# Performance work log

Hardware: AMD Instinct MI355X
Metric: run time of the kernel (lower is better)

## Reference

```python
import jax, jax.numpy as jnp
import numpy as np

B, N, H, HEADS, F, L = 32, 256, 512, 8, 2048, 8
D = H // HEADS  # per-head dim
EPS = 1e-5


def _layernorm(x, scale, bias):
    mu = jnp.mean(x, axis=-1, keepdims=True)
    var = jnp.mean(jnp.square(x - mu), axis=-1, keepdims=True)
    return (x - mu) * jax.lax.rsqrt(var + EPS) * scale + bias


def setup_inputs() -> dict:
    key = jax.random.key(0)
    ks = jax.random.split(key, 12)
    s = 0.02
    inp = {
        "x": jax.random.normal(ks[0], (B, N, H), jnp.float32),
        "attn_bias": jax.random.normal(ks[1], (B, HEADS, N, N), jnp.float32),
        "ln1_s": jnp.ones((L, H), jnp.float32),
        "ln1_b": jnp.zeros((L, H), jnp.float32),
        "wq": s * jax.random.normal(ks[2], (L, H, H), jnp.float32),
        "bq": jnp.zeros((L, H), jnp.float32),
        "wk": s * jax.random.normal(ks[3], (L, H, H), jnp.float32),
        "bk": jnp.zeros((L, H), jnp.float32),
        "wv": s * jax.random.normal(ks[4], (L, H, H), jnp.float32),
        "bv": jnp.zeros((L, H), jnp.float32),
        "wo": s * jax.random.normal(ks[5], (L, H, H), jnp.float32),
        "bo": jnp.zeros((L, H), jnp.float32),
        "ln2_s": jnp.ones((L, H), jnp.float32),
        "ln2_b": jnp.zeros((L, H), jnp.float32),
        "w1": s * jax.random.normal(ks[6], (L, H, F), jnp.float32),
        "b1": jnp.zeros((L, F), jnp.float32),
        "w2": s * jax.random.normal(ks[7], (L, F, H), jnp.float32),
        "b2": jnp.zeros((L, H), jnp.float32),
    }
    return inp


def reference(x, attn_bias, ln1_s, ln1_b, wq, bq, wk, bk, wv, bv, wo, bo,
              ln2_s, ln2_b, w1, b1, w2, b2):
    scale = D ** (-0.5)
    for l in range(L):
        # --- self attention block ---
        y = _layernorm(x, ln1_s[l], ln1_b[l])
        q = (y @ wq[l] + bq[l]).reshape(B, N, HEADS, D) * scale
        k = (y @ wk[l] + bk[l]).reshape(B, N, HEADS, D)
        v = (y @ wv[l] + bv[l]).reshape(B, N, HEADS, D)
        scores = jnp.einsum("bqhd,bkhd->bhqk", q, k) + attn_bias
        probs = jax.nn.softmax(scores, axis=-1)
        ctx = jnp.einsum("bhqk,bkhd->bqhd", probs, v).reshape(B, N, H)
        x = x + ctx @ wo[l] + bo[l]
        # --- FFN block ---
        y = _layernorm(x, ln2_s[l], ln2_b[l])
        y = jax.nn.gelu(y @ w1[l] + b1[l], approximate=False)
        x = x + y @ w2[l] + b2[l]
    return x
```

## Files before the change

### kernel.cpp

```cpp
#include <hip/hip_runtime.h>
#include <hip/hip_bf16.h>
#include <math.h>

typedef __bf16 bf16;
typedef __bf16 bf16x8 __attribute__((ext_vector_type(8)));
typedef float  f32x4  __attribute__((ext_vector_type(4)));

#define DEV __device__ __forceinline__

DEV f32x4 mfma16(bf16x8 a, bf16x8 b, f32x4 c) {
    return __builtin_amdgcn_mfma_f32_16x16x32_bf16(a, b, c, 0, 0, 0);
}

template <int MODE>
__global__ __launch_bounds__(256, 2) void gemm_k(
    const bf16* __restrict__ A, const bf16* __restrict__ Bt,
    const float* __restrict__ bias, bf16* __restrict__ Cb,
    float* __restrict__ Cf, int K, int ldC)
{
    __shared__ bf16 As[128 * 32];
    __shared__ bf16 Bs[128 * 32];
    const int tid  = threadIdx.x;
    const int lane = tid & 63;
    const int w    = tid >> 6;
    const int wm   = w & 1, wn = w >> 1;
    const long tm  = (long)blockIdx.y * 128;
    const long tn  = (long)blockIdx.x * 128;

    f32x4 acc[4][4] = {};

    const int p0 = tid, p1 = tid + 256;
    const int r0 = p0 >> 2, c0 = (p0 & 3) * 8;
    const int r1 = p1 >> 2, c1 = (p1 & 3) * 8;
    const bf16* A0 = A + (tm + r0) * K + c0;
    const bf16* A1 = A + (tm + r1) * K + c1;
    const bf16* B0 = Bt + (tn + r0) * K + c0;
    const bf16* B1 = Bt + (tn + r1) * K + c1;

    int am[4], bn[4];
#pragma unroll
    for (int i = 0; i < 4; ++i) {
        int ra = wm * 64 + i * 16 + (lane & 15);
        am[i]  = ra * 32 + (lane >> 4) * 8;
        int rb = wn * 64 + i * 16 + (lane & 15);
        bn[i]  = rb * 32 + (lane >> 4) * 8;
    }

    for (int k0 = 0; k0 < K; k0 += 32) {
        uint4 va0 = *(const uint4*)(A0 + k0);
        uint4 va1 = *(const uint4*)(A1 + k0);
        uint4 vb0 = *(const uint4*)(B0 + k0);
        uint4 vb1 = *(const uint4*)(B1 + k0);
        __syncthreads();
        *(uint4*)&As[p0 * 8] = va0;
        *(uint4*)&As[p1 * 8] = va1;
        *(uint4*)&Bs[p0 * 8] = vb0;
        *(uint4*)&Bs[p1 * 8] = vb1;
        __syncthreads();
        bf16x8 a[4], b[4];
#pragma unroll
        for (int i = 0; i < 4; ++i) a[i] = *(const bf16x8*)&As[am[i]];
#pragma unroll
        for (int i = 0; i < 4; ++i) b[i] = *(const bf16x8*)&Bs[bn[i]];
#pragma unroll
        for (int mi = 0; mi < 4; ++mi)
#pragma unroll
            for (int ni = 0; ni < 4; ++ni)
                acc[mi][ni] = mfma16(a[mi], b[ni], acc[mi][ni]);
    }

#pragma unroll
    for (int mi = 0; mi < 4; ++mi) {
        const long rbase = tm + wm * 64 + mi * 16 + ((lane >> 4) << 2);
#pragma unroll
        for (int ni = 0; ni < 4; ++ni) {
            const long col = tn + wn * 64 + ni * 16 + (lane & 15);
            const float bv = bias[col];
#pragma unroll
            for (int r = 0; r < 4; ++r) {
                float v = acc[mi][ni][r] + bv;
                if constexpr (MODE == 1)
                    v = 0.5f * v * (1.0f + erff(v * 0.70710678118654752f));
                const long idx = (rbase + r) * (long)ldC + col;
                if constexpr (MODE == 2) Cf[idx] += v;
                else                     Cb[idx] = (bf16)v;
            }
        }
    }
}

__global__ __launch_bounds__(256, 2) void attn_k(
    const bf16* __restrict__ qkv, const float* __restrict__ bias,
    bf16* __restrict__ ctx)
{
    __shared__ bf16 smem[256 * 72 + 32 * 264];
    bf16* Ks = smem;
    bf16* Vt = smem + 256 * 72;

    const int tid = threadIdx.x, lane = tid & 63, w = tid >> 6;
    const int qt = blockIdx.x & 3;
    const int h  = (blockIdx.x >> 2) & 7;
    const int b  = blockIdx.x >> 5;
    const long qkv_base = (long)b * 256 * 1536;

#pragma unroll
    for (int i = 0; i < 8; ++i) {
        int p = i * 256 + tid;
        int n = p >> 3, kk = (p & 7) * 8;
        uint4 v = *(const uint4*)(qkv + qkv_base + (long)n * 1536 + 512 + h * 64 + kk);
        *(uint4*)&Ks[n * 72 + kk] = v;
    }
    {
        int d = tid & 31, nb = tid >> 5;
#pragma unroll 4
        for (int i = 0; i < 32; ++i) {
            int n = nb + i * 8;
            Vt[d * 264 + n] = qkv[qkv_base + (long)n * 1536 + 1024 + h * 64 + d];
        }
    }

    const int qr0 = qt * 64 + w * 16;
    bf16x8 aq0, aq1;
    {
        const bf16* g = qkv + qkv_base + (long)(qr0 + (lane & 15)) * 1536 + h * 64 + ((lane >> 4) * 8);
        aq0 = *(const bf16x8*)g;
        aq1 = *(const bf16x8*)(g + 32);
    }
    __syncthreads();

    f32x4 s[16];
    const float* bb = bias + (((long)(b * 8 + h)) * 256 + qr0) * 256;
#pragma unroll
    for (int ct = 0; ct < 16; ++ct) {
        const int col = ct * 16 + (lane & 15);
        f32x4 c;
#pragma unroll
        for (int r = 0; r < 4; ++r)
            c[r] = bb[(long)((lane >> 4) * 4 + r) * 256 + col];
        bf16x8 k0 = *(const bf16x8*)&Ks[(ct * 16 + (lane & 15)) * 72 + ((lane >> 4) * 8)];
        bf16x8 k1 = *(const bf16x8*)&Ks[(ct * 16 + (lane & 15)) * 72 + 32 + ((lane >> 4) * 8)];
        c = mfma16(aq0, k0, c);
        c = mfma16(aq1, k1, c);
        s[ct] = c;
    }

    float m[4] = {-1e30f, -1e30f, -1e30f, -1e30f};
#pragma unroll
    for (int ct = 0; ct < 16; ++ct)
#pragma unroll
        for (int r = 0; r < 4; ++r) m[r] = fmaxf(m[r], s[ct][r]);
#pragma unroll
    for (int r = 0; r < 4; ++r)
#pragma unroll
        for (int off = 1; off < 16; off <<= 1)
            m[r] = fmaxf(m[r], __shfl_xor(m[r], off));
    float l[4] = {0.f, 0.f, 0.f, 0.f};
#pragma unroll
    for (int ct = 0; ct < 16; ++ct)
#pragma unroll
        for (int r = 0; r < 4; ++r) {
            float p = __expf(s[ct][r] - m[r]);
            s[ct][r] = p;
            l[r] += p;
        }
#pragma unroll
    for (int r = 0; r < 4; ++r) {
#pragma unroll
        for (int off = 1; off < 16; off <<= 1) l[r] += __shfl_xor(l[r], off);
        l[r] = 1.0f / l[r];
    }

    __syncthreads();
    bf16* P = Ks + w * (16 * 264);
#pragma unroll
    for (int ct = 0; ct < 16; ++ct)
#pragma unroll
        for (int r = 0; r < 4; ++r)
            P[(long)((lane >> 4) * 4 + r) * 264 + ct * 16 + (lane & 15)] = (bf16)s[ct][r];

    bf16x8 ap[8];
#pragma unroll
    for (int nk = 0; nk < 8; ++nk)
        ap[nk] = *(const bf16x8*)&P[(lane & 15) * 264 + nk * 32 + (lane >> 4) * 8];

    f32x4 o[4];
#pragma unroll
    for (int dt = 0; dt < 2; ++dt) {
        f32x4 c = {};
#pragma unroll
        for (int nk = 0; nk < 8; ++nk) {
            bf16x8 bv = *(const bf16x8*)&Vt[(dt * 16 + (lane & 15)) * 264 + nk * 32 + (lane >> 4) * 8];
            c = mfma16(ap[nk], bv, c);
        }
        o[dt] = c;
    }

    __syncthreads();
    {
        int d = tid & 31, nb = tid >> 5;
#pragma unroll 4
        for (int i = 0; i < 32; ++i) {
            int n = nb + i * 8;
            Vt[d * 264 + n] = qkv[qkv_base + (long)n * 1536 + 1024 + h * 64 + 32 + d];
        }
    }
    __syncthreads();
#pragma unroll
    for (int dt = 0; dt < 2; ++dt) {
        f32x4 c = {};
#pragma unroll
        for (int nk = 0; nk < 8; ++nk) {
            bf16x8 bv = *(const bf16x8*)&Vt[(dt * 16 + (lane & 15)) * 264 + nk * 32 + (lane >> 4) * 8];
            c = mfma16(ap[nk], bv, c);
        }
        o[2 + dt] = c;
    }

#pragma unroll
    for (int dt = 0; dt < 4; ++dt) {
        const int col = h * 64 + dt * 16 + (lane & 15);
#pragma unroll
        for (int r = 0; r < 4; ++r) {
            const long row = (long)b * 256 + qr0 + (lane >> 4) * 4 + r;
            ctx[row * 512 + col] = (bf16)(o[dt][r] * l[r]);
        }
    }
}

__global__ __launch_bounds__(256) void ln_k(
    const float* __restrict__ x, const float* __restrict__ sc,
    const float* __restrict__ bi, bf16* __restrict__ y)
{
    const int lane = threadIdx.x & 63;
    const long row = (long)blockIdx.x * 4 + (threadIdx.x >> 6);
    const float* xr = x + row * 512;
    float v[8];
    *(float4*)&v[0] = ((const float4*)xr)[lane * 2];
    *(float4*)&v[4] = ((const float4*)xr)[lane * 2 + 1];
    float sum = 0.f;
#pragma unroll
    for (int j = 0; j < 8; ++j) sum += v[j];
#pragma unroll
    for (int off = 1; off < 64; off <<= 1) sum += __shfl_xor(sum, off);
    const float mu = sum * (1.0f / 512.0f);
    float sq = 0.f;
#pragma unroll
    for (int j = 0; j < 8; ++j) { float d = v[j] - mu; sq += d * d; }
#pragma unroll
    for (int off = 1; off < 64; off <<= 1) sq += __shfl_xor(sq, off);
    const float rs = rsqrtf(sq * (1.0f / 512.0f) + 1e-5f);
    bf16* yr = y + row * 512;
#pragma unroll
    for (int j = 0; j < 8; ++j) {
        int c = lane * 8 + j;
        yr[c] = (bf16)((v[j] - mu) * rs * sc[c] + bi[c]);
    }
}

__global__ __launch_bounds__(256) void transpose_k(
    const float* __restrict__ wq, const float* __restrict__ wk,
    const float* __restrict__ wv, const float* __restrict__ wo,
    const float* __restrict__ w1, const float* __restrict__ w2,
    bf16* __restrict__ qkvT, bf16* __restrict__ woT,
    bf16* __restrict__ w1T, bf16* __restrict__ w2T)
{
    __shared__ float tile[32][33];
    const int tid = threadIdx.x, tx = tid & 31, ty = tid >> 5;
    const int l = blockIdx.x / 3072;
    const int r = blockIdx.x % 3072;

    const float* In = nullptr;
    bf16* Out = nullptr;
    int Nd, tk, tn, rowOff = 0, ldO;
    float scale = 1.0f;
    if (r < 1024) {
        const int which = r >> 8, t = r & 255;
        tn = t >> 4; tk = t & 15; Nd = 512; ldO = 512;
        const long woff = (long)l * 512 * 512;
        if (which == 0)      { In = wq + woff; Out = qkvT + (long)l * 1536 * 512; rowOff = 0;    scale = 0.125f; }
        else if (which == 1) { In = wk + woff; Out = qkvT + (long)l * 1536 * 512; rowOff = 512;  }
        else if (which == 2) { In = wv + woff; Out = qkvT + (long)l * 1536 * 512; rowOff = 1024; }
        else                 { In = wo + woff; Out = woT + woff; }
    } else if (r < 2048) {
        const int t = r - 1024;
        tn = t >> 4; tk = t & 15; Nd = 2048; ldO = 512;
        In = w1 + (long)l * 512 * 2048; Out = w1T + (long)l * 2048 * 512;
    } else {
        const int t = r - 2048;
        tn = t & 15; tk = t >> 4; Nd = 512; ldO = 2048;
        In = w2 + (long)l * 2048 * 512; Out = w2T + (long)l * 512 * 2048;
    }
    const int gk = tk * 32, gn = tn * 32;
#pragma unroll
    for (int j = 0; j < 4; ++j) {
        int rr = ty + j * 8;
        tile[rr][tx] = In[(long)(gk + rr) * Nd + gn + tx] * scale;
    }
    __syncthreads();
#pragma unroll
    for (int j = 0; j < 4; ++j) {
        int rr = ty + j * 8;
        Out[(long)(rowOff + gn + rr) * ldO + gk + tx] = (bf16)tile[tx][rr];
    }
}

__global__ void biasq_k(const float* __restrict__ bq, const float* __restrict__ bk,
                        const float* __restrict__ bv, float* __restrict__ bqkv)
{
    int i = blockIdx.x * 256 + threadIdx.x;
    if (i >= 8 * 1536) return;
    int l = i / 1536, j = i % 1536;
    float v;
    if (j < 512)       v = bq[l * 512 + j] * 0.125f;
    else if (j < 1024) v = bk[l * 512 + j - 512];
    else               v = bv[l * 512 + j - 1024];
    bqkv[i] = v;
}

extern "C" void kernel_launch(void* const* d_in, const int* in_sizes, int n_in,
                              void* d_out, int out_size, void* d_ws, size_t ws_size,
                              hipStream_t stream)
{
    (void)in_sizes; (void)n_in; (void)out_size; (void)ws_size;
    const float* x    = (const float*)d_in[0];
    const float* ab   = (const float*)d_in[1];
    const float* ln1s = (const float*)d_in[2];
    const float* ln1b = (const float*)d_in[3];
    const float* wq   = (const float*)d_in[4];
    const float* bq   = (const float*)d_in[5];
    const float* wk   = (const float*)d_in[6];
    const float* bk   = (const float*)d_in[7];
    const float* wv   = (const float*)d_in[8];
    const float* bv   = (const float*)d_in[9];
    const float* wo   = (const float*)d_in[10];
    const float* bo   = (const float*)d_in[11];
    const float* ln2s = (const float*)d_in[12];
    const float* ln2b = (const float*)d_in[13];
    const float* w1   = (const float*)d_in[14];
    const float* b1   = (const float*)d_in[15];
    const float* w2   = (const float*)d_in[16];
    const float* b2   = (const float*)d_in[17];

    char* ws = (char*)d_ws;
    float* xf   = (float*)ws;
    bf16* y     = (bf16*)(ws + 16777216);
    bf16* ctx   = y;
    bf16* qkv   = (bf16*)(ws + 16777216 + 8388608);
    bf16* ffn   = qkv;
    bf16* wqkvT = (bf16*)(ws + 16777216 + 8388608 + 33554432);
    bf16* woT   = wqkvT + (long)8 * 1536 * 512;
    bf16* w1T   = woT + (long)8 * 512 * 512;
    bf16* w2T   = w1T + (long)8 * 2048 * 512;
    float* bqkv = (float*)(w2T + (long)8 * 512 * 2048);

    hipMemcpyAsync(xf, x, (size_t)8192 * 512 * 4, hipMemcpyDeviceToDevice, stream);
    transpose_k<<<24576, 256, 0, stream>>>(wq, wk, wv, wo, w1, w2, wqkvT, woT, w1T, w2T);
    biasq_k<<<48, 256, 0, stream>>>(bq, bk, bv, bqkv);

    for (int l = 0; l < 8; ++l) {
        ln_k<<<2048, 256, 0, stream>>>(xf, ln1s + l * 512, ln1b + l * 512, y);
        gemm_k<0><<<dim3(12, 64), 256, 0, stream>>>(
            y, wqkvT + (long)l * 1536 * 512, bqkv + l * 1536, qkv, nullptr, 512, 1536);
        attn_k<<<1024, 256, 0, stream>>>(qkv, ab, ctx);
        gemm_k<2><<<dim3(4, 64), 256, 0, stream>>>(
            ctx, woT + (long)l * 512 * 512, bo + l * 512, nullptr, xf, 512, 512);
        ln_k<<<2048, 256, 0, stream>>>(xf, ln2s + l * 512, ln2b + l * 512, y);
        gemm_k<1><<<dim3(16, 64), 256, 0, stream>>>(
            y, w1T + (long)l * 2048 * 512, b1 + l * 2048, ffn, nullptr, 512, 2048);
        gemm_k<2><<<dim3(4, 64), 256, 0, stream>>>(
            ffn, w2T + (long)l * 512 * 2048, b2 + l * 512, nullptr, xf, 2048, 512);
    }
    hipMemcpyAsync(d_out, xf, (size_t)8192 * 512 * 4, hipMemcpyDeviceToDevice, stream);
}
```

Measured before the change: 1.615 ms.

## Split-K residual GEMMs with atomics, swizzle LDS, prefetch next K tile

The two residual GEMMs (out-projection and FFN down-projection) now split K across blockIdx.z slices and accumulate into the fp32 residual with atomicAdd, with only slice 0 adding the bias. The aim is more blocks for these narrow N=512 GEMMs, which launched only 256 blocks before. The shared-memory tiles are XOR-swizzled to reduce bank conflicts, and global loads for the next K tile are issued before the MFMA work so they overlap compute. Costs include atomic traffic, nondeterministic summation order, and extra registers held for the prefetched data.

```diff
diff --git a/kernel.cpp b/kernel.cpp
--- a/kernel.cpp
+++ b/kernel.cpp
@@ -16,7 +16,7 @@
 __global__ __launch_bounds__(256, 2) void gemm_k(
     const bf16* __restrict__ A, const bf16* __restrict__ Bt,
     const float* __restrict__ bias, bf16* __restrict__ Cb,
-    float* __restrict__ Cf, int K, int ldC)
+    float* __restrict__ Cf, int K, int Ks, int ldC)
 {
     __shared__ bf16 As[128 * 32];
     __shared__ bf16 Bs[128 * 32];
@@ -26,37 +26,48 @@
     const int wm   = w & 1, wn = w >> 1;
     const long tm  = (long)blockIdx.y * 128;
     const long tn  = (long)blockIdx.x * 128;
+    const int slice = blockIdx.z;
+    const int kbase = slice * Ks;
 
     f32x4 acc[4][4] = {};
 
     const int p0 = tid, p1 = tid + 256;
     const int r0 = p0 >> 2, c0 = (p0 & 3) * 8;
     const int r1 = p1 >> 2, c1 = (p1 & 3) * 8;
-    const bf16* A0 = A + (tm + r0) * K + c0;
-    const bf16* A1 = A + (tm + r1) * K + c1;
-    const bf16* B0 = Bt + (tn + r0) * K + c0;
-    const bf16* B1 = Bt + (tn + r1) * K + c1;
+    const int s0 = r0 * 32 + (((p0 & 3) ^ ((r0 >> 1) & 3)) * 8);
+    const int s1 = r1 * 32 + (((p1 & 3) ^ ((r1 >> 1) & 3)) * 8);
+    const bf16* A0 = A + (tm + r0) * K + kbase + c0;
+    const bf16* A1 = A + (tm + r1) * K + kbase + c1;
+    const bf16* B0 = Bt + (tn + r0) * K + kbase + c0;
+    const bf16* B1 = Bt + (tn + r1) * K + kbase + c1;
 
     int am[4], bn[4];
 #pragma unroll
     for (int i = 0; i < 4; ++i) {
         int ra = wm * 64 + i * 16 + (lane & 15);
-        am[i]  = ra * 32 + (lane >> 4) * 8;
+        am[i]  = ra * 32 + (((lane >> 4) ^ ((ra >> 1) & 3)) * 8);
         int rb = wn * 64 + i * 16 + (lane & 15);
-        bn[i]  = rb * 32 + (lane >> 4) * 8;
-    }
-
-    for (int k0 = 0; k0 < K; k0 += 32) {
-        uint4 va0 = *(const uint4*)(A0 + k0);
-        uint4 va1 = *(const uint4*)(A1 + k0);
-        uint4 vb0 = *(const uint4*)(B0 + k0);
-        uint4 vb1 = *(const uint4*)(B1 + k0);
+        bn[i]  = rb * 32 + (((lane >> 4) ^ ((rb >> 1) & 3)) * 8);
+    }
+
+    uint4 va0 = *(const uint4*)A0;
+    uint4 va1 = *(const uint4*)A1;
+    uint4 vb0 = *(const uint4*)B0;
+    uint4 vb1 = *(const uint4*)B1;
+
+    for (int k0 = 0; k0 < Ks; k0 += 32) {
         __syncthreads();
-        *(uint4*)&As[p0 * 8] = va0;
-        *(uint4*)&As[p1 * 8] = va1;
-        *(uint4*)&Bs[p0 * 8] = vb0;
-        *(uint4*)&Bs[p1 * 8] = vb1;
+        *(uint4*)&As[s0] = va0;
+        *(uint4*)&As[s1] = va1;
+        *(uint4*)&Bs[s0] = vb0;
+        *(uint4*)&Bs[s1] = vb1;
         __syncthreads();
+        if (k0 + 32 < Ks) {
+            va0 = *(const uint4*)(A0 + k0 + 32);
+            va1 = *(const uint4*)(A1 + k0 + 32);
+            vb0 = *(const uint4*)(B0 + k0 + 32);
+            vb1 = *(const uint4*)(B1 + k0 + 32);
+        }
         bf16x8 a[4], b[4];
 #pragma unroll
         for (int i = 0; i < 4; ++i) a[i] = *(const bf16x8*)&As[am[i]];
@@ -75,14 +86,14 @@
 #pragma unroll
         for (int ni = 0; ni < 4; ++ni) {
             const long col = tn + wn * 64 + ni * 16 + (lane & 15);
-            const float bv = bias[col];
+            const float bv = (MODE == 3 && slice != 0) ? 0.f : bias[col];
 #pragma unroll
             for (int r = 0; r < 4; ++r) {
                 float v = acc[mi][ni][r] + bv;
                 if constexpr (MODE == 1)
                     v = 0.5f * v * (1.0f + erff(v * 0.70710678118654752f));
                 const long idx = (rbase + r) * (long)ldC + col;
-                if constexpr (MODE == 2) Cf[idx] += v;
+                if constexpr (MODE == 3) atomicAdd(&Cf[idx], v);
                 else                     Cb[idx] = (bf16)v;
             }
         }
@@ -359,16 +370,16 @@
 
     for (int l = 0; l < 8; ++l) {
         ln_k<<<2048, 256, 0, stream>>>(xf, ln1s + l * 512, ln1b + l * 512, y);
-        gemm_k<0><<<dim3(12, 64), 256, 0, stream>>>(
-            y, wqkvT + (long)l * 1536 * 512, bqkv + l * 1536, qkv, nullptr, 512, 1536);
+        gemm_k<0><<<dim3(12, 64, 1), 256, 0, stream>>>(
+            y, wqkvT + (long)l * 1536 * 512, bqkv + l * 1536, qkv, nullptr, 512, 512, 1536);
         attn_k<<<1024, 256, 0, stream>>>(qkv, ab, ctx);
-        gemm_k<2><<<dim3(4, 64), 256, 0, stream>>>(
-            ctx, woT + (long)l * 512 * 512, bo + l * 512, nullptr, xf, 512, 512);
+        gemm_k<3><<<dim3(4, 64, 2), 256, 0, stream>>>(
+            ctx, woT + (long)l * 512 * 512, bo + l * 512, nullptr, xf, 512, 256, 512);
         ln_k<<<2048, 256, 0, stream>>>(xf, ln2s + l * 512, ln2b + l * 512, y);
-        gemm_k<1><<<dim3(16, 64), 256, 0, stream>>>(
-            y, w1T + (long)l * 2048 * 512, b1 + l * 2048, ffn, nullptr, 512, 2048);
-        gemm_k<2><<<dim3(4, 64), 256, 0, stream>>>(
-            ffn, w2T + (long)l * 512 * 2048, b2 + l * 512, nullptr, xf, 2048, 512);
+        gemm_k<1><<<dim3(16, 64, 1), 256, 0, stream>>>(
+            y, w1T + (long)l * 2048 * 512, b1 + l * 2048, ffn, nullptr, 512, 512, 2048);
+        gemm_k<3><<<dim3(4, 64, 4), 256, 0, stream>>>(
+            ffn, w2T + (long)l * 512 * 2048, b2 + l * 512, nullptr, xf, 2048, 512, 512);
     }
     hipMemcpyAsync(d_out, xf, (size_t)8192 * 512 * 4, hipMemcpyDeviceToDevice, stream);
 }
```

After: 1.801 ms. +11.5%, slower.
